# Performance work log

Hardware: AMD Instinct MI355X
Metric: run time of the kernel (lower is better)

The kernel has to match this reference:

```python
import jax, jax.numpy as jnp
import numpy as np

N_NODES = 20000
N_EDGES = 160000
N_GRAPHS = 500
F_IN = 128
HID = 512
N_CLS = 10
N_LAYERS = 3
BN_EPS = 1e-5
BN_BIAS = 1e-4  # BatchNorm1d weight init to 1, bias to 0.0001


def bn(x):
    # training-mode BatchNorm1d with gamma=1, beta=1e-4 (per module init)
    m = jnp.mean(x, axis=0)
    v = jnp.mean((x - m) ** 2, axis=0)
    return (x - m) * jax.lax.rsqrt(v + BN_EPS) + BN_BIAS


def gcn_norm(row, col, edge_weight, num_nodes):
    # add self loops with weight 1, symmetric deg^-1/2 normalization
    loop = jnp.arange(num_nodes)
    r = jnp.concatenate([row, loop])
    c = jnp.concatenate([col, loop])
    w = jnp.concatenate([edge_weight, jnp.ones((num_nodes,), edge_weight.dtype)])
    deg = jax.ops.segment_sum(w, r, num_segments=num_nodes)
    dis = jnp.where(deg > 0, jax.lax.rsqrt(deg), jnp.zeros_like(deg))
    return r, c, dis[r] * w * dis[c]


def gcn(x, W, b, r, c, norm):
    # x@W then gather source feats, scale by norm, scatter-add to targets
    h = x @ W
    out = jax.ops.segment_sum(norm[:, None] * h[c], r, num_segments=x.shape[0])
    return out + b


def readout(x, W1, b1, W2, b2):
    x = bn(x) @ W1 + b1
    x = jax.nn.relu(x)
    x = bn(x) @ W2 + b2
    return jax.nn.log_softmax(x, axis=-1)


def setup_inputs() -> dict:
    key = jax.random.key(0)
    ks = iter(jax.random.split(key, 40))

    def lin(k, fin, fout):
        return jax.random.normal(k, (fin, fout), jnp.float32) * (1.0 / np.sqrt(fin))

    x = jax.random.normal(next(ks), (N_NODES, F_IN), jnp.float32)
    edge_index = jax.random.randint(next(ks), (2, N_EDGES), 0, N_NODES)
    batch = jnp.sort(jax.random.randint(next(ks), (N_NODES,), 0, N_GRAPHS))
    perm = jax.random.permutation(next(ks), N_GRAPHS)

    inp = {"x": x, "edge_index": edge_index, "batch": batch, "perm": perm}
    inp["conv_feat_W"] = lin(next(ks), F_IN, HID)
    inp["conv_feat_b"] = jnp.zeros((HID,), jnp.float32)
    inp["convs_W"] = jax.random.normal(next(ks), (N_LAYERS, HID, HID), jnp.float32) * (1.0 / np.sqrt(HID))
    inp["convs_b"] = jnp.zeros((N_LAYERS, HID), jnp.float32)
    inp["edge_att_W"] = lin(next(ks), 2 * HID, 2)
    inp["edge_att_b"] = jnp.zeros((2,), jnp.float32)
    inp["node_att_W"] = lin(next(ks), HID, 2)
    inp["node_att_b"] = jnp.zeros((2,), jnp.float32)
    inp["ctx_W"] = lin(next(ks), HID, HID)
    inp["ctx_b"] = jnp.zeros((HID,), jnp.float32)
    inp["obj_W"] = lin(next(ks), HID, HID)
    inp["obj_b"] = jnp.zeros((HID,), jnp.float32)
    for tag in ("c", "o", "co"):
        inp[f"fc1_{tag}_W"] = lin(next(ks), HID, HID)
        inp[f"fc1_{tag}_b"] = jnp.zeros((HID,), jnp.float32)
        inp[f"fc2_{tag}_W"] = lin(next(ks), HID, N_CLS)
        inp[f"fc2_{tag}_b"] = jnp.zeros((N_CLS,), jnp.float32)
    return inp


def reference(x, edge_index, batch, perm,
              conv_feat_W, conv_feat_b, convs_W, convs_b,
              edge_att_W, edge_att_b, node_att_W, node_att_b,
              ctx_W, ctx_b, obj_W, obj_b,
              fc1_c_W, fc1_c_b, fc2_c_W, fc2_c_b,
              fc1_o_W, fc1_o_b, fc2_o_W, fc2_o_b,
              fc1_co_W, fc1_co_b, fc2_co_W, fc2_co_b):
    row, col = edge_index[0], edge_index[1]
    n = x.shape[0]

    x = bn(x)
    x = jax.nn.relu(x @ conv_feat_W + conv_feat_b)  # conv_feat has gfn=True: pure linear

    # unweighted symmetric norm, shared by all stacked convs
    r1, c1, nrm1 = gcn_norm(row, col, jnp.ones((row.shape[0],), x.dtype), n)
    for i in range(N_LAYERS):
        x = bn(x)
        x = jax.nn.relu(gcn(x, convs_W[i], convs_b[i], r1, c1, nrm1))

    edge_rep = jnp.concatenate([x[row], x[col]], axis=-1)        # [E, 2H]
    edge_att = jax.nn.softmax(edge_rep @ edge_att_W + edge_att_b, axis=-1)
    node_att = jax.nn.softmax(x @ node_att_W + node_att_b, axis=-1)

    xc = node_att[:, :1] * x
    xo = node_att[:, 1:] * x

    rc, cc, nc = gcn_norm(row, col, edge_att[:, 0], n)
    ro, co_, no_ = gcn_norm(row, col, edge_att[:, 1], n)
    xc = jax.nn.relu(gcn(bn(xc), ctx_W, ctx_b, rc, cc, nc))
    xo = jax.nn.relu(gcn(bn(xo), obj_W, obj_b, ro, co_, no_))

    xc = jax.ops.segment_sum(xc, batch, num_segments=N_GRAPHS)   # global_add_pool
    xo = jax.ops.segment_sum(xo, batch, num_segments=N_GRAPHS)

    xc_logis = readout(xc, fc1_c_W, fc1_c_b, fc2_c_W, fc2_c_b)
    xo_logis = readout(xo, fc1_o_W, fc1_o_b, fc2_o_W, fc2_o_b)
    # cat_or_add == 'add', with_random shuffle realized by perm
    xco_logis = readout(xc[perm] + xo, fc1_co_W, fc1_co_b, fc2_co_W, fc2_co_b)
    return xc_logis, xo_logis, xco_logis
```

## Files before the change

### kernel.cpp

```cpp
#include <hip/hip_runtime.h>
#include <stdint.h>

#define NN 20000
#define NE 160000
#define NG 500
#define FIN 128
#define HID 512
#define NCLS 10
#define BNG 256
#define NB3 32

typedef __attribute__((ext_vector_type(8))) short short8;
typedef __attribute__((ext_vector_type(4))) float f32x4;
typedef __attribute__((ext_vector_type(4))) unsigned short ushort4v;

__device__ __forceinline__ float bf2f(unsigned int u){
  union{unsigned int i; float f;} x; x.i = u<<16; return x.f;
}
__device__ __forceinline__ unsigned short f2bf(float f){
  union{float f; unsigned int i;} x; x.f=f;
  unsigned int r = x.i + 0x7fffu + ((x.i>>16)&1u);
  return (unsigned short)(r>>16);
}
__device__ __forceinline__ unsigned int pk2(float a, float b){
  return (unsigned int)f2bf(a) | ((unsigned int)f2bf(b) << 16);
}

__device__ __forceinline__ void gload16(unsigned short* lds, const unsigned short* g){
  __builtin_amdgcn_global_load_lds((const __attribute__((address_space(1))) unsigned int*)g,
                                   (__attribute__((address_space(3))) unsigned int*)lds,
                                   16, 0, 0);
}

__device__ __forceinline__ void fma8(float* acc, uint4 v, float w){
  acc[0] += w*bf2f(v.x & 0xffffu); acc[1] += w*bf2f(v.x >> 16);
  acc[2] += w*bf2f(v.y & 0xffffu); acc[3] += w*bf2f(v.y >> 16);
  acc[4] += w*bf2f(v.z & 0xffffu); acc[5] += w*bf2f(v.z >> 16);
  acc[6] += w*bf2f(v.w & 0xffffu); acc[7] += w*bf2f(v.w >> 16);
}

__global__ void sentinel_k(float* out){ out[0] = 12345.0f; }

struct W2BT { const float* src[9]; unsigned short* dst[9]; };
__global__ void setup_all(W2BT p, int* __restrict__ cnt, int* __restrict__ fillc,
                          float* __restrict__ degc, float* __restrict__ dego,
                          float* __restrict__ Sc, float* __restrict__ So,
                          float* __restrict__ stats6){
  int idx = blockIdx.x*blockDim.x + threadIdx.x;
  if (idx < FIN*HID + 8*HID*HID){
    int seg, off, K;
    if (idx < FIN*HID){ seg = 0; off = idx; K = FIN; }
    else {
      int r = idx - FIN*HID;
      seg = 1 + (r >> 18); off = r & (HID*HID-1); K = HID;
    }
    int k = off >> 9, n = off & 511;
    p.dst[seg][(size_t)n*K + k] = f2bf(p.src[seg][off]);
  }
  if (idx < NN){ cnt[idx]=0; fillc[idx]=0; degc[idx]=1.0f; dego[idx]=1.0f; Sc[idx]=0.f; So[idx]=0.f; }
  if (idx < 6*1024) stats6[idx] = 0.f;
}

__global__ __launch_bounds__(1024) void bnstats_p(const float* __restrict__ X, int M, int F,
                                                  float* __restrict__ partials){
  __shared__ float lds[1024*9];
  const int t = threadIdx.x;
  const int cg = F >> 2;
  const int cid = t & (cg-1);
  const int rid = t / cg;
  const int rpb = 1024 / cg;
  float s0=0,s1=0,s2=0,s3=0,q0=0,q1=0,q2=0,q3=0;
  const int rowsPer = (M + BNG - 1)/BNG;
  int r0 = blockIdx.x*rowsPer, r1 = r0 + rowsPer; if (r1 > M) r1 = M;
  for (int r = r0 + rid; r < r1; r += rpb){
    float4 v = *(const float4*)&X[(size_t)r*F + cid*4];
    s0+=v.x; q0+=v.x*v.x; s1+=v.y; q1+=v.y*v.y; s2+=v.z; q2+=v.z*v.z; s3+=v.w; q3+=v.w*v.w;
  }
  int base = (rid*cg + cid)*9;
  lds[base+0]=s0; lds[base+1]=s1; lds[base+2]=s2; lds[base+3]=s3;
  lds[base+4]=q0; lds[base+5]=q1; lds[base+6]=q2; lds[base+7]=q3;
  __syncthreads();
  if (t < cg*8){
    int ci = t >> 3, i = t & 7;
    float acc = 0.f;
    for (int g=0; g<rpb; ++g) acc += lds[(g*cg + ci)*9 + i];
    int col = ci*4 + (i & 3);
    partials[(size_t)blockIdx.x*(2*F) + ((i < 4) ? col : F + col)] = acc;
  }
}

__global__ __launch_bounds__(1024) void bnstats_dual(const unsigned short* __restrict__ X,
                                                     const float* __restrict__ na,
                                                     float* __restrict__ partials){
  __shared__ float lds[1024*17];
  const int t = threadIdx.x;
  const int cid = t & 127;
  const int rid = t >> 7;
  float sC[4]={0,0,0,0}, qC[4]={0,0,0,0}, sO[4]={0,0,0,0}, qO[4]={0,0,0,0};
  const int rowsPer = (NN + BNG - 1)/BNG;
  int r0 = blockIdx.x*rowsPer, r1 = r0 + rowsPer; if (r1 > NN) r1 = NN;
  for (int r = r0 + rid; r < r1; r += 8){
    float a0 = na[2*r], a1 = na[2*r+1];
    uint2 u = *(const uint2*)&X[(size_t)r*HID + cid*4];
    float e[4] = {bf2f(u.x & 0xffffu), bf2f(u.x >> 16), bf2f(u.y & 0xffffu), bf2f(u.y >> 16)};
#pragma unroll
    for (int i=0;i<4;i++){
      float vc = e[i]*a0, vo = e[i]*a1;
      sC[i]+=vc; qC[i]+=vc*vc; sO[i]+=vo; qO[i]+=vo*vo;
    }
  }
  int base = (rid*128 + cid)*17;
#pragma unroll
  for (int i=0;i<4;i++){
    lds[base+i]=sC[i]; lds[base+4+i]=qC[i]; lds[base+8+i]=sO[i]; lds[base+12+i]=qO[i];
  }
  __syncthreads();
  for (int idx = t; idx < 2048; idx += 1024){
    int ci = idx >> 4, i = idx & 15;
    float acc = 0.f;
    for (int g=0; g<8; ++g) acc += lds[(g*128 + ci)*17 + i];
    int grp = i >> 2, col = ci*4 + (i & 3);
    partials[(size_t)blockIdx.x*2048 + grp*HID + col] = acc;
  }
}

__global__ void bnfin_red(const float* __restrict__ partials, int stride, int off,
                          int M, int F, float* __restrict__ mstat){
  __shared__ float lds[4][64][2];
  int t = threadIdx.x;
  int cl = t & 63, ch = t >> 6;
  int c = blockIdx.x*64 + cl;
  float s = 0.f, q = 0.f;
  if (c < F){
    for (int b = ch*64; b < ch*64 + 64; ++b){
      s += partials[(size_t)b*stride + off + c];
      q += partials[(size_t)b*stride + off + F + c];
    }
  }
  lds[ch][cl][0] = s; lds[ch][cl][1] = q;
  __syncthreads();
  if (ch == 0 && c < F){
    s = lds[0][cl][0]+lds[1][cl][0]+lds[2][cl][0]+lds[3][cl][0];
    q = lds[0][cl][1]+lds[1][cl][1]+lds[2][cl][1]+lds[3][cl][1];
    float m = s/(float)M;
    float v = q/(float)M - m*m;
    mstat[c] = m;
    mstat[F+c] = rsqrtf(v + 1e-5f);
  }
}

__global__ void bnfin_red2(const float* __restrict__ partials, float* __restrict__ mstatCO){
  __shared__ float lds[4][64][2];
  int t = threadIdx.x;
  int cl = t & 63, ch = t >> 6;
  int c = blockIdx.x*64 + cl;
  int off = blockIdx.y*1024;
  float s = 0.f, q = 0.f;
  for (int b = ch*64; b < ch*64 + 64; ++b){
    s += partials[(size_t)b*2048 + off + c];
    q += partials[(size_t)b*2048 + off + HID + c];
  }
  lds[ch][cl][0] = s; lds[ch][cl][1] = q;
  __syncthreads();
  if (ch == 0){
    s = lds[0][cl][0]+lds[1][cl][0]+lds[2][cl][0]+lds[3][cl][0];
    q = lds[0][cl][1]+lds[1][cl][1]+lds[2][cl][1]+lds[3][cl][1];
    float m = s/(float)NN;
    float v = q/(float)NN - m*m;
    mstatCO[blockIdx.y*1024 + c] = m;
    mstatCO[blockIdx.y*1024 + HID + c] = rsqrtf(v + 1e-5f);
  }
}

__global__ void bncast(const float* __restrict__ X, const float* __restrict__ mstat,
                       int M, int F, unsigned short* __restrict__ out){
  int idx = blockIdx.x*blockDim.x + threadIdx.x;
  int total4 = M*F/4;
  if (idx >= total4) return;
  int base = idx*4;
  int c = base & (F-1);
  float4 v = *(const float4*)&X[base];
  ushort4v o;
  o[0] = f2bf((v.x - mstat[c+0])*mstat[F+c+0] + 1e-4f);
  o[1] = f2bf((v.y - mstat[c+1])*mstat[F+c+1] + 1e-4f);
  o[2] = f2bf((v.z - mstat[c+2])*mstat[F+c+2] + 1e-4f);
  o[3] = f2bf((v.w - mstat[c+3])*mstat[F+c+3] + 1e-4f);
  *(ushort4v*)&out[base] = o;
}

__global__ void csr_count(const int* __restrict__ ei, int* __restrict__ cnt){
  int e = blockIdx.x*blockDim.x + threadIdx.x;
  if (e < NE) atomicAdd(&cnt[ei[e]], 1);
}

__global__ __launch_bounds__(1024) void scan1(const int* __restrict__ cnt, int* __restrict__ rowp,
                                              float* __restrict__ dis1, int* __restrict__ bsum){
  __shared__ int buf[1024];
  int t = threadIdx.x;
  int i = blockIdx.x*1024 + t;
  int v = 0;
  if (i < NN){ v = cnt[i] + 1; dis1[i] = rsqrtf((float)v); }
  buf[t] = v;
  __syncthreads();
  for (int off=1; off<1024; off<<=1){
    int xv = (t >= off) ? buf[t-off] : 0;
    __syncthreads();
    buf[t] += xv;
    __syncthreads();
  }
  if (i < NN) rowp[i+1] = buf[t];
  if (t == 1023) bsum[blockIdx.x] = buf[1023];
}

__global__ __launch_bounds__(1024) void scan3(int* __restrict__ rowp, const int* __restrict__ bsum){
  __shared__ int base;
  int bx = blockIdx.x;
  if (threadIdx.x == 0){
    int a = 0;
    for (int b=0; b<bx; ++b) a += bsum[b];
    base = a;
  }
  __syncthreads();
  int i = bx*1024 + threadIdx.x;
  if (i < NN) rowp[i+1] += base;
  if (i == 0) rowp[0] = 0;
}

__global__ void csr_fill(const int* __restrict__ ei, const int* __restrict__ rowp,
                         const int* __restrict__ cnt, int* __restrict__ fillc,
                         const float* __restrict__ dis1,
                         int* __restrict__ ccol, int* __restrict__ crow, int* __restrict__ ceid,
                         float* __restrict__ w1){
  int id = blockIdx.x*blockDim.x + threadIdx.x;
  if (id < NE){
    int r = ei[id], c = ei[NE + id];
    int pos = atomicAdd(&fillc[r], 1);
    int idx = rowp[r] + pos;
    ccol[idx] = c; crow[idx] = r; ceid[idx] = id;
    w1[idx] = dis1[r]*dis1[c];
  } else if (id < NE + NN){
    int i = id - NE;
    int idx = rowp[i] + cnt[i];
    ccol[idx] = i; crow[idx] = i; ceid[idx] = -1;
    w1[idx] = dis1[i]*dis1[i];
  }
}

__global__ void att_node(const unsigned short* __restrict__ X, const float* __restrict__ nW,
                         const float* __restrict__ nb, const float* __restrict__ eW,
                         float* __restrict__ na, float* __restrict__ eab){
  int wv = blockIdx.x*4 + (threadIdx.x >> 6);
  int l = threadIdx.x & 63;
  if (wv >= NN) return;
  uint4 u = ((const uint4*)(X + (size_t)wv*HID))[l];
  float xv[8] = {bf2f(u.x&0xffffu), bf2f(u.x>>16), bf2f(u.y&0xffffu), bf2f(u.y>>16),
                 bf2f(u.z&0xffffu), bf2f(u.z>>16), bf2f(u.w&0xffffu), bf2f(u.w>>16)};
  float s0=0,s1=0,s2=0,s3=0,s4=0,s5=0;
#pragma unroll
  for (int j=0; j<8; ++j){
    int k = l*8 + j;
    float x = xv[j];
    s0 += x * nW[2*k];       s1 += x * nW[2*k+1];
    s2 += x * eW[2*k];       s3 += x * eW[2*k+1];
    s4 += x * eW[2*(512+k)]; s5 += x * eW[2*(512+k)+1];
  }
  for (int m=1; m<64; m<<=1){
    s0 += __shfl_xor(s0,m); s1 += __shfl_xor(s1,m); s2 += __shfl_xor(s2,m);
    s3 += __shfl_xor(s3,m); s4 += __shfl_xor(s4,m); s5 += __shfl_xor(s5,m);
  }
  if (l == 0){
    float z0 = s0 + nb[0], z1 = s1 + nb[1];
    float mx = fmaxf(z0,z1);
    float e0 = expf(z0-mx), e1 = expf(z1-mx);
    float inv = 1.0f/(e0+e1);
    na[2*wv] = e0*inv; na[2*wv+1] = e1*inv;
    eab[4*wv] = s2; eab[4*wv+1] = s3; eab[4*wv+2] = s4; eab[4*wv+3] = s5;
  }
}

__global__ void att_edge(const int* __restrict__ ei, const float* __restrict__ eab,
                         const float* __restrict__ eb, float* __restrict__ att,
                         float* __restrict__ degc, float* __restrict__ dego){
  int e = blockIdx.x*blockDim.x + threadIdx.x;
  if (e >= NE) return;
  int r = ei[e], c = ei[NE+e];
  float z0 = eab[4*r]   + eab[4*c+2] + eb[0];
  float z1 = eab[4*r+1] + eab[4*c+3] + eb[1];
  float mx = fmaxf(z0,z1);
  float e0 = expf(z0-mx), e1 = expf(z1-mx);
  float inv = 1.0f/(e0+e1);
  float a0 = e0*inv, a1 = e1*inv;
  att[2*e] = a0; att[2*e+1] = a1;
  atomicAdd(&degc[r], a0);
  atomicAdd(&dego[r], a1);
}

__global__ void wco_kernel(const int* __restrict__ crow, const int* __restrict__ ccol,
                           const int* __restrict__ ceid, const float* __restrict__ att,
                           const float* __restrict__ degc, const float* __restrict__ dego,
                           const float* __restrict__ na,
                           float* __restrict__ wcv, float* __restrict__ wov,
                           float* __restrict__ Sc, float* __restrict__ So){
  int j = blockIdx.x*blockDim.x + threadIdx.x;
  if (j >= NE + NN) return;
  int r = crow[j], c = ccol[j], e = ceid[j];
  float a0 = (e < 0) ? 1.0f : att[2*e];
  float a1 = (e < 0) ? 1.0f : att[2*e+1];
  float wc = rsqrtf(degc[r]) * a0 * rsqrtf(degc[c]);
  float wo = rsqrtf(dego[r]) * a1 * rsqrtf(dego[c]);
  wcv[j] = wc * na[2*c];
  wov[j] = wo * na[2*c+1];
  atomicAdd(&Sc[r], wc);
  atomicAdd(&So[r], wo);
}

__global__ __launch_bounds__(256) void aggregate_bn(const unsigned short* __restrict__ A,
                                                    const int* __restrict__ rowp,
                                                    const int* __restrict__ ccol,
                                                    const float* __restrict__ wv,
                                                    const float* __restrict__ stats,
                                                    float invM,
                                                    unsigned short* __restrict__ out){
  int row = blockIdx.x*4 + (threadIdx.x >> 6);
  int l = threadIdx.x & 63;
  const uint4* Av = (const uint4*)A;
  int s = rowp[row], e = rowp[row+1];
  float acc[8] = {0,0,0,0,0,0,0,0};
  float sw = 0.f;
  int j = s;
  for (; j+1 < e; j += 2){
    int c0 = ccol[j], c1 = ccol[j+1];
    float w0 = wv[j], w1 = wv[j+1];
    uint4 v0 = Av[(size_t)c0*64 + l];
    uint4 v1 = Av[(size_t)c1*64 + l];
    fma8(acc, v0, w0);
    fma8(acc, v1, w1);
    sw += w0 + w1;
  }
  if (j < e){
    uint4 v = Av[(size_t)ccol[j]*64 + l];
    fma8(acc, v, wv[j]);
    sw += wv[j];
  }
  float g[8];
#pragma unroll
  for (int i=0;i<8;i++){
    int c = l*8 + i;
    float m = stats[c]*invM;
    float rs = rsqrtf(stats[512+c]*invM - m*m + 1e-5f);
    g[i] = rs*acc[i] + sw*(1e-4f - m*rs);
  }
  uint4 o;
  o.x = pk2(g[0],g[1]); o.y = pk2(g[2],g[3]); o.z = pk2(g[4],g[5]); o.w = pk2(g[6],g[7]);
  ((uint4*)out)[(size_t)row*64 + l] = o;
}

__global__ __launch_bounds__(256) void aggregate_dual(const unsigned short* __restrict__ A,
                                                      const int* __restrict__ rowp,
                                                      const int* __restrict__ ccol,
                                                      const float* __restrict__ wc,
                                                      const float* __restrict__ wo,
                                                      const float* __restrict__ Sc,
                                                      const float* __restrict__ So,
                                                      const float* __restrict__ mstatCO,
                                                      unsigned short* __restrict__ outC,
                                                      unsigned short* __restrict__ outO){
  int row = blockIdx.x*4 + (threadIdx.x >> 6);
  int l = threadIdx.x & 63;
  const uint4* Av = (const uint4*)A;
  int s = rowp[row], e = rowp[row+1];
  float aC[8] = {0,0,0,0,0,0,0,0};
  float aO[8] = {0,0,0,0,0,0,0,0};
  int j = s;
  for (; j+1 < e; j += 2){
    int c0 = ccol[j], c1 = ccol[j+1];
    float wc0 = wc[j], wc1 = wc[j+1];
    float wo0 = wo[j], wo1 = wo[j+1];
    uint4 v0 = Av[(size_t)c0*64 + l];
    uint4 v1 = Av[(size_t)c1*64 + l];
    fma8(aC, v0, wc0); fma8(aO, v0, wo0);
    fma8(aC, v1, wc1); fma8(aO, v1, wo1);
  }
  if (j < e){
    uint4 v = Av[(size_t)ccol[j]*64 + l];
    fma8(aC, v, wc[j]); fma8(aO, v, wo[j]);
  }
  float ScR = Sc[row], SoR = So[row];
  float gC[8], gO[8];
#pragma unroll
  for (int i=0;i<8;i++){
    int c = l*8 + i;
    float mc = mstatCO[c],      rc = mstatCO[512+c];
    float mo = mstatCO[1024+c], ro = mstatCO[1536+c];
    gC[i] = rc*aC[i] + ScR*(1e-4f - mc*rc);
    gO[i] = ro*aO[i] + SoR*(1e-4f - mo*ro);
  }
  uint4 oc, oo;
  oc.x = pk2(gC[0],gC[1]); oc.y = pk2(gC[2],gC[3]); oc.z = pk2(gC[4],gC[5]); oc.w = pk2(gC[6],gC[7]);
  oo.x = pk2(gO[0],gO[1]); oo.y = pk2(gO[2],gO[3]); oo.z = pk2(gO[4],gO[5]); oo.w = pk2(gO[6],gO[7]);
  ((uint4*)outC)[(size_t)row*64 + l] = oc;
  ((uint4*)outO)[(size_t)row*64 + l] = oo;
}

__global__ __launch_bounds__(256) void gemm_bt(const unsigned short* __restrict__ A,
                                               const unsigned short* __restrict__ Bt,
                                               unsigned short* __restrict__ O,
                                               const float* __restrict__ bias,
                                               float* __restrict__ stats,
                                               int M, int K, int relu){
  __shared__ unsigned short As[2][128*32];
  __shared__ unsigned short Bs[2][128*32];
  const int tid = threadIdx.x;
  const int w = tid >> 6, l = tid & 63;
  const int m0 = blockIdx.x*128, n0 = blockIdx.y*128;
  const int wm = w >> 1, wn = w & 1;
  const int lr = l & 15, lh = l >> 4;

  f32x4 acc[4][4];
#pragma unroll
  for (int i=0;i<4;i++)
#pragma unroll
    for (int j=0;j<4;j++) acc[i][j] = 0.0f;

  const int q0 = w*2, q1 = w*2+1;
  const int sub = l >> 2;
  const int kc  = (l & 3)*8;
  int ma0 = m0 + q0*16 + sub; if (ma0 >= M) ma0 = M-1;
  int ma1 = m0 + q1*16 + sub; if (ma1 >= M) ma1 = M-1;
  const int nb0 = n0 + q0*16 + sub;
  const int nb1 = n0 + q1*16 + sub;
  const unsigned short* Ar0 = A + (size_t)ma0*K + kc;
  const unsigned short* Ar1 = A + (size_t)ma1*K + kc;
  const unsigned short* Br0 = Bt + (size_t)nb0*K + kc;
  const unsigned short* Br1 = Bt + (size_t)nb1*K + kc;

  const int NT = K >> 5;
  gload16(&As[0][q0*512], Ar0);
  gload16(&As[0][q1*512], Ar1);
  gload16(&Bs[0][q0*512], Br0);
  gload16(&Bs[0][q1*512], Br1);
  __syncthreads();
  int cur = 0;
  for (int t=0; t<NT; ++t){
    if (t+1 < NT){
      int k1 = (t+1) << 5;
      gload16(&As[cur^1][q0*512], Ar0 + k1);
      gload16(&As[cur^1][q1*512], Ar1 + k1);
      gload16(&Bs[cur^1][q0*512], Br0 + k1);
      gload16(&Bs[cur^1][q1*512], Br1 + k1);
    }
    short8 af[4], bfr[4];
#pragma unroll
    for (int fm=0; fm<4; ++fm) af[fm]  = *(const short8*)&As[cur][(wm*64 + fm*16 + lr)*32 + lh*8];
#pragma unroll
    for (int fn=0; fn<4; ++fn) bfr[fn] = *(const short8*)&Bs[cur][(wn*64 + fn*16 + lr)*32 + lh*8];
#pragma unroll
    for (int fm=0; fm<4; ++fm)
#pragma unroll
      for (int fn=0; fn<4; ++fn)
        acc[fm][fn] = __builtin_amdgcn_mfma_f32_16x16x32_bf16(af[fm], bfr[fn], acc[fm][fn], 0, 0, 0);
    __syncthreads();
    cur ^= 1;
  }
  float bv[4], cs[4]={0,0,0,0}, cq[4]={0,0,0,0};
  int col[4];
#pragma unroll
  for (int fn=0; fn<4; ++fn){ col[fn] = n0 + wn*64 + fn*16 + lr; bv[fn] = bias[col[fn]]; }
#pragma unroll
  for (int fm=0; fm<4; ++fm){
#pragma unroll
    for (int j=0; j<4; ++j){
      int row = m0 + wm*64 + fm*16 + lh*4 + j;
      if (row < M){
#pragma unroll
        for (int fn=0; fn<4; ++fn){
          float v = acc[fm][fn][j] + bv[fn];
          if (relu) v = fmaxf(v, 0.f);
          O[(size_t)row*HID + col[fn]] = f2bf(v);
          cs[fn] += v; cq[fn] += v*v;
        }
      }
    }
  }
  if (stats){
#pragma unroll
    for (int m=16; m<64; m<<=1){
#pragma unroll
      for (int fn=0; fn<4; ++fn){ cs[fn] += __shfl_xor(cs[fn], m); cq[fn] += __shfl_xor(cq[fn], m); }
    }
    if (lh == 0){
#pragma unroll
      for (int fn=0; fn<4; ++fn){
        atomicAdd(&stats[col[fn]], cs[fn]);
        atomicAdd(&stats[512+col[fn]], cq[fn]);
      }
    }
  }
}

struct FC1P { const unsigned short* Bt[3]; const float* bias[3]; };
__global__ __launch_bounds__(256) void gemm_fc1(const unsigned short* __restrict__ A, FC1P p,
                                                unsigned short* __restrict__ O,
                                                float* __restrict__ statsB){
  __shared__ unsigned short As[2][128*32];
  __shared__ unsigned short Bs[2][128*32];
  const int tid = threadIdx.x;
  const int w = tid >> 6, l = tid & 63;
  const int m0 = blockIdx.x*128, n0 = blockIdx.y*128;
  const int branch = blockIdx.x >> 2;
  const unsigned short* Bt = p.Bt[branch];
  const float* bias = p.bias[branch];
  float* stats = statsB + branch*1024;
  const int K = HID;
  const int wm = w >> 1, wn = w & 1;
  const int lr = l & 15, lh = l >> 4;

  f32x4 acc[4][4];
#pragma unroll
  for (int i=0;i<4;i++)
#pragma unroll
    for (int j=0;j<4;j++) acc[i][j] = 0.0f;

  const int q0 = w*2, q1 = w*2+1;
  const int sub = l >> 2;
  const int kc  = (l & 3)*8;
  const int ma0 = m0 + q0*16 + sub;
  const int ma1 = m0 + q1*16 + sub;
  const int nb0 = n0 + q0*16 + sub;
  const int nb1 = n0 + q1*16 + sub;
  const unsigned short* Ar0 = A + (size_t)ma0*K + kc;
  const unsigned short* Ar1 = A + (size_t)ma1*K + kc;
  const unsigned short* Br0 = Bt + (size_t)nb0*K + kc;
  const unsigned short* Br1 = Bt + (size_t)nb1*K + kc;

  const int NT = K >> 5;
  gload16(&As[0][q0*512], Ar0);
  gload16(&As[0][q1*512], Ar1);
  gload16(&Bs[0][q0*512], Br0);
  gload16(&Bs[0][q1*512], Br1);
  __syncthreads();
  int cur = 0;
  for (int t=0; t<NT; ++t){
    if (t+1 < NT){
      int k1 = (t+1) << 5;
      gload16(&As[cur^1][q0*512], Ar0 + k1);
      gload16(&As[cur^1][q1*512], Ar1 + k1);
      gload16(&Bs[cur^1][q0*512], Br0 + k1);
      gload16(&Bs[cur^1][q1*512], Br1 + k1);
    }
    short8 af[4], bfr[4];
#pragma unroll
    for (int fm=0; fm<4; ++fm) af[fm]  = *(const short8*)&As[cur][(wm*64 + fm*16 + lr)*32 + lh*8];
#pragma unroll
    for (int fn=0; fn<4; ++fn) bfr[fn] = *(const short8*)&Bs[cur][(wn*64 + fn*16 + lr)*32 + lh*8];
#pragma unroll
    for (int fm=0; fm<4; ++fm)
#pragma unroll
      for (int fn=0; fn<4; ++fn)
        acc[fm][fn] = __builtin_amdgcn_mfma_f32_16x16x32_bf16(af[fm], bfr[fn], acc[fm][fn], 0, 0, 0);
    __syncthreads();
    cur ^= 1;
  }
  float bv[4], cs[4]={0,0,0,0}, cq[4]={0,0,0,0};
  int col[4];
#pragma unroll
  for (int fn=0; fn<4; ++fn){ col[fn] = n0 + wn*64 + fn*16 + lr; bv[fn] = bias[col[fn]]; }
#pragma unroll
  for (int fm=0; fm<4; ++fm){
#pragma unroll
    for (int j=0; j<4; ++j){
      int row = m0 + wm*64 + fm*16 + lh*4 + j;
      bool real = (row & 511) < NG;
#pragma unroll
      for (int fn=0; fn<4; ++fn){
        float v = fmaxf(acc[fm][fn][j] + bv[fn], 0.f);
        O[(size_t)row*HID + col[fn]] = f2bf(v);
        if (real){ cs[fn] += v; cq[fn] += v*v; }
      }
    }
  }
#pragma unroll
  for (int m=16; m<64; m<<=1){
#pragma unroll
    for (int fn=0; fn<4; ++fn){ cs[fn] += __shfl_xor(cs[fn], m); cq[fn] += __shfl_xor(cq[fn], m); }
  }
  if (lh == 0){
#pragma unroll
    for (int fn=0; fn<4; ++fn){
      atomicAdd(&stats[col[fn]], cs[fn]);
      atomicAdd(&stats[512+col[fn]], cq[fn]);
    }
  }
}

__global__ void pool2(const unsigned short* __restrict__ XC, const unsigned short* __restrict__ XO,
                      const int* __restrict__ batch, float* __restrict__ gc, float* __restrict__ go){
  int g = blockIdx.x;
  int t = threadIdx.x;
  const unsigned short* X = blockIdx.y ? XO : XC;
  float* out = blockIdx.y ? go : gc;
  int lo = 0, hi = NN;
  while (lo < hi){ int mid = (lo+hi) >> 1; if (batch[mid] < g) lo = mid+1; else hi = mid; }
  int s = lo;
  lo = 0; hi = NN;
  while (lo < hi){ int mid = (lo+hi) >> 1; if (batch[mid] < g+1) lo = mid+1; else hi = mid; }
  int e = lo;
  float a0 = 0.f, a1 = 0.f;
  for (int i=s; i<e; ++i){
    unsigned int v = *(const unsigned int*)&X[(size_t)i*HID + t*2];
    a0 += bf2f(v & 0xffffu); a1 += bf2f(v >> 16);
  }
  out[(size_t)g*HID + t*2]     = a0;
  out[(size_t)g*HID + t*2 + 1] = a1;
}

__global__ __launch_bounds__(256) void bnstats3(const float* __restrict__ gc, const float* __restrict__ go,
                                                const int* __restrict__ perm, float* __restrict__ partials){
  __shared__ float lds[256*9];
  int br = blockIdx.y;
  int t = threadIdx.x;
  int cid = t & 127, rid = t >> 7;
  float s[4]={0,0,0,0}, q[4]={0,0,0,0};
  const int rowsPer = (NG + NB3 - 1)/NB3;
  int r0 = blockIdx.x*rowsPer, r1 = r0 + rowsPer; if (r1 > NG) r1 = NG;
  for (int r = r0 + rid; r < r1; r += 2){
    float4 v;
    if (br == 0)      v = *(const float4*)&gc[(size_t)r*HID + cid*4];
    else if (br == 1) v = *(const float4*)&go[(size_t)r*HID + cid*4];
    else {
      int ps = perm[r];
      float4 a = *(const float4*)&gc[(size_t)ps*HID + cid*4];
      float4 b = *(const float4*)&go[(size_t)r*HID + cid*4];
      v = make_float4(a.x+b.x, a.y+b.y, a.z+b.z, a.w+b.w);
    }
    float e[4] = {v.x, v.y, v.z, v.w};
#pragma unroll
    for (int i=0;i<4;i++){ s[i]+=e[i]; q[i]+=e[i]*e[i]; }
  }
  int base = (rid*128 + cid)*9;
#pragma unroll
  for (int i=0;i<4;i++){ lds[base+i]=s[i]; lds[base+4+i]=q[i]; }
  __syncthreads();
  for (int o = t; o < 1024; o += 256){
    int issq = o >> 9, col = o & 511;
    int ci = col >> 2, i = col & 3;
    float acc = lds[(0*128 + ci)*9 + issq*4 + i] + lds[(1*128 + ci)*9 + issq*4 + i];
    partials[(size_t)(br*NB3 + blockIdx.x)*1024 + issq*512 + col] = acc;
  }
}

__global__ void bnfin3(const float* __restrict__ partials, float* __restrict__ mstat3){
  __shared__ float lds[4][64][2];
  int t = threadIdx.x;
  int cl = t & 63, ch = t >> 6;
  int c = blockIdx.x*64 + cl;
  int br = blockIdx.y;
  float s = 0.f, q = 0.f;
  for (int b = ch*8; b < ch*8 + 8; ++b){
    s += partials[(size_t)(br*NB3 + b)*1024 + c];
    q += partials[(size_t)(br*NB3 + b)*1024 + 512 + c];
  }
  lds[ch][cl][0] = s; lds[ch][cl][1] = q;
  __syncthreads();
  if (ch == 0){
    s = lds[0][cl][0]+lds[1][cl][0]+lds[2][cl][0]+lds[3][cl][0];
    q = lds[0][cl][1]+lds[1][cl][1]+lds[2][cl][1]+lds[3][cl][1];
    float m = s/(float)NG;
    float v = q/(float)NG - m*m;
    mstat3[br*1024 + c] = m;
    mstat3[br*1024 + 512 + c] = rsqrtf(v + 1e-5f);
  }
}

__global__ void bncast3(const float* __restrict__ gc, const float* __restrict__ go,
                        const int* __restrict__ perm, const float* __restrict__ mstat3,
                        unsigned short* __restrict__ out){
  int idx = blockIdx.x*blockDim.x + threadIdx.x;
  if (idx >= 1536*128) return;
  int r = idx >> 7;
  int cg = idx & 127;
  int br = r >> 9, lr = r & 511;
  ushort4v o;
  if (lr >= NG){ o[0]=0; o[1]=0; o[2]=0; o[3]=0; }
  else {
    float4 v;
    if (br == 0)      v = *(const float4*)&gc[(size_t)lr*HID + cg*4];
    else if (br == 1) v = *(const float4*)&go[(size_t)lr*HID + cg*4];
    else {
      int ps = perm[lr];
      float4 a = *(const float4*)&gc[(size_t)ps*HID + cg*4];
      float4 b = *(const float4*)&go[(size_t)lr*HID + cg*4];
      v = make_float4(a.x+b.x, a.y+b.y, a.z+b.z, a.w+b.w);
    }
    const float* ms = mstat3 + br*1024;
    int c = cg*4;
    o[0] = f2bf((v.x - ms[c+0])*ms[512+c+0] + 1e-4f);
    o[1] = f2bf((v.y - ms[c+1])*ms[512+c+1] + 1e-4f);
    o[2] = f2bf((v.z - ms[c+2])*ms[512+c+2] + 1e-4f);
    o[3] = f2bf((v.w - ms[c+3])*ms[512+c+3] + 1e-4f);
  }
  *(ushort4v*)&out[(size_t)r*HID + cg*4] = o;
}

struct ROP { const float* W2[3]; const float* b2[3]; };
__global__ void readout_final3(const unsigned short* __restrict__ T, const float* __restrict__ statsB,
                               float invM, ROP p, float* __restrict__ out){
  int g = blockIdx.x;
  int br = blockIdx.y;
  int l = threadIdx.x;
  const float* stats = statsB + br*1024;
  const float* W2 = p.W2[br];
  const float* b2 = p.b2[br];
  float acc[NCLS];
#pragma unroll
  for (int c=0; c<NCLS; ++c) acc[c] = 0.f;
  uint4 u = ((const uint4*)(T + (size_t)(br*512 + g)*HID))[l];
  float xv[8] = {bf2f(u.x&0xffffu), bf2f(u.x>>16), bf2f(u.y&0xffffu), bf2f(u.y>>16),
                 bf2f(u.z&0xffffu), bf2f(u.z>>16), bf2f(u.w&0xffffu), bf2f(u.w>>16)};
#pragma unroll
  for (int j=0; j<8; ++j){
    int k = l*8 + j;
    float m = stats[k]*invM;
    float rs = rsqrtf(stats[512+k]*invM - m*m + 1e-5f);
    float v = (xv[j] - m)*rs + 1e-4f;
#pragma unroll
    for (int c=0; c<NCLS; ++c) acc[c] += v * W2[k*NCLS + c];
  }
  for (int m=1; m<64; m<<=1){
#pragma unroll
    for (int c=0; c<NCLS; ++c) acc[c] += __shfl_xor(acc[c], m);
  }
  if (l == 0){
    float z[NCLS];
    float mx = -1e30f;
#pragma unroll
    for (int c=0; c<NCLS; ++c){ z[c] = acc[c] + b2[c]; mx = fmaxf(mx, z[c]); }
    float s = 0.f;
#pragma unroll
    for (int c=0; c<NCLS; ++c) s += expf(z[c]-mx);
    float lse = mx + logf(s);
#pragma unroll
    for (int c=0; c<NCLS; ++c) out[(size_t)(br*NG + g)*NCLS + c] = z[c] - lse;
  }
}

extern "C" void kernel_launch(void* const* d_in, const int* in_sizes, int n_in,
                              void* d_out, int out_size, void* d_ws, size_t ws_size,
                              hipStream_t stream){
  (void)in_sizes; (void)n_in; (void)out_size;
  const float* x      = (const float*)d_in[0];
  const int*   ei     = (const int*)d_in[1];
  const int*   batch  = (const int*)d_in[2];
  const int*   perm   = (const int*)d_in[3];
  const float* convfW = (const float*)d_in[4];
  const float* convfB = (const float*)d_in[5];
  const float* convsW = (const float*)d_in[6];
  const float* convsB = (const float*)d_in[7];
  const float* eattW  = (const float*)d_in[8];
  const float* eattB  = (const float*)d_in[9];
  const float* nattW  = (const float*)d_in[10];
  const float* nattB  = (const float*)d_in[11];
  const float* ctxW   = (const float*)d_in[12];
  const float* ctxB   = (const float*)d_in[13];
  const float* objW   = (const float*)d_in[14];
  const float* objB   = (const float*)d_in[15];
  const float* fc1W[3] = {(const float*)d_in[16], (const float*)d_in[20], (const float*)d_in[24]};
  const float* fc1B[3] = {(const float*)d_in[17], (const float*)d_in[21], (const float*)d_in[25]};
  const float* fc2W[3] = {(const float*)d_in[18], (const float*)d_in[22], (const float*)d_in[26]};
  const float* fc2B[3] = {(const float*)d_in[19], (const float*)d_in[23], (const float*)d_in[27]};
  float* out = (float*)d_out;

  char* p = (char*)d_ws;
  auto alloc = [&](size_t bytes)->char*{ char* r = p; p += (bytes + 255) & ~((size_t)255); return r; };
  const int T = NE + NN;
  unsigned short* Xbf = (unsigned short*)alloc((size_t)NN*HID*2);
  unsigned short* Gbf = (unsigned short*)alloc((size_t)NN*HID*2);
  unsigned short* GbfO= (unsigned short*)alloc((size_t)NN*HID*2);
  unsigned short* Abf = (unsigned short*)alloc((size_t)NN*FIN*2);
  unsigned short* WtF = (unsigned short*)alloc((size_t)HID*FIN*2);
  unsigned short* WtL = (unsigned short*)alloc((size_t)3*HID*HID*2);
  unsigned short* WtC = (unsigned short*)alloc((size_t)HID*HID*2);
  unsigned short* WtO = (unsigned short*)alloc((size_t)HID*HID*2);
  unsigned short* WtR = (unsigned short*)alloc((size_t)3*HID*HID*2);
  int* cnt   = (int*)alloc((size_t)NN*4);
  int* fillc = (int*)alloc((size_t)NN*4);
  int* rowp  = (int*)alloc((size_t)(NN+1)*4);
  int* bsum  = (int*)alloc(32*4);
  int* ccol  = (int*)alloc((size_t)T*4);
  int* crow  = (int*)alloc((size_t)T*4);
  int* ceid  = (int*)alloc((size_t)T*4);
  float* w1  = (float*)alloc((size_t)T*4);
  float* wcv = (float*)alloc((size_t)T*4);
  float* wov = (float*)alloc((size_t)T*4);
  float* dis1 = (float*)alloc((size_t)NN*4);
  float* degc = (float*)alloc((size_t)NN*4);
  float* dego = (float*)alloc((size_t)NN*4);
  float* Sc   = (float*)alloc((size_t)NN*4);
  float* So   = (float*)alloc((size_t)NN*4);
  float* stats6 = (float*)alloc(6*1024*4);
  float* mstat  = (float*)alloc(2*HID*4);
  float* mstatCO= (float*)alloc(2*1024*4);
  float* mstat3 = (float*)alloc(3*1024*4);
  float* na   = (float*)alloc((size_t)NN*2*4);
  float* eab  = (float*)alloc((size_t)NN*4*4);
  float* att  = (float*)alloc((size_t)NE*2*4);
  float* gc   = (float*)alloc((size_t)NG*HID*4);
  float* go   = (float*)alloc((size_t)NG*HID*4);
  float* part = (float*)alloc((size_t)BNG*2048*4);
  if ((size_t)(p - (char*)d_ws) > ws_size){
    sentinel_k<<<1,1,0,stream>>>(out);
    return;
  }
  unsigned short* Abf3 = Abf;
  unsigned short* Gbf3 = GbfO;
  const float invNN = 1.0f/(float)NN;
  const float invNG = 1.0f/(float)NG;

  W2BT wp;
  wp.src[0]=convfW; wp.dst[0]=WtF;
  for (int i=0;i<3;i++){ wp.src[1+i]=convsW+(size_t)i*HID*HID; wp.dst[1+i]=WtL+(size_t)i*HID*HID; }
  wp.src[4]=ctxW; wp.dst[4]=WtC;
  wp.src[5]=objW; wp.dst[5]=WtO;
  for (int i=0;i<3;i++){ wp.src[6+i]=fc1W[i]; wp.dst[6+i]=WtR+(size_t)i*HID*HID; }
  setup_all<<<(FIN*HID + 8*HID*HID + 255)/256, 256, 0, stream>>>(wp, cnt, fillc, degc, dego, Sc, So, stats6);

  csr_count<<<(NE+255)/256,256,0,stream>>>(ei, cnt);
  scan1<<<(NN+1023)/1024,1024,0,stream>>>(cnt, rowp, dis1, bsum);
  scan3<<<(NN+1023)/1024,1024,0,stream>>>(rowp, bsum);
  csr_fill<<<(T+255)/256,256,0,stream>>>(ei, rowp, cnt, fillc, dis1, ccol, crow, ceid, w1);

  bnstats_p<<<BNG,1024,0,stream>>>(x, NN, FIN, part);
  bnfin_red<<<(FIN+63)/64,256,0,stream>>>(part, 2*FIN, 0, NN, FIN, mstat);
  bncast<<<((NN*FIN/4)+255)/256,256,0,stream>>>(x, mstat, NN, FIN, Abf);
  gemm_bt<<<dim3((NN+127)/128,4),256,0,stream>>>(Abf, WtF, Xbf, convfB, stats6, NN, FIN, 1);

  for (int i=0;i<3;i++){
    aggregate_bn<<<NN/4,256,0,stream>>>(Xbf, rowp, ccol, w1, stats6 + i*1024, invNN, Gbf);
    gemm_bt<<<dim3((NN+127)/128,4),256,0,stream>>>(Gbf, WtL+(size_t)i*HID*HID, Xbf,
                                                   convsB+(size_t)i*HID,
                                                   (i<2) ? (stats6 + (i+1)*1024) : nullptr,
                                                   NN, HID, 1);
  }

  att_node<<<(NN+3)/4,256,0,stream>>>(Xbf, nattW, nattB, eattW, na, eab);
  att_edge<<<(NE+255)/256,256,0,stream>>>(ei, eab, eattB, att, degc, dego);
  wco_kernel<<<(T+255)/256,256,0,stream>>>(crow, ccol, ceid, att, degc, dego, na, wcv, wov, Sc, So);

  bnstats_dual<<<BNG,1024,0,stream>>>(Xbf, na, part);
  bnfin_red2<<<dim3(8,2),256,0,stream>>>(part, mstatCO);
  aggregate_dual<<<NN/4,256,0,stream>>>(Xbf, rowp, ccol, wcv, wov, Sc, So, mstatCO, Gbf, GbfO);
  gemm_bt<<<dim3((NN+127)/128,4),256,0,stream>>>(Gbf, WtC, Xbf, ctxB, nullptr, NN, HID, 1);
  gemm_bt<<<dim3((NN+127)/128,4),256,0,stream>>>(GbfO, WtO, Gbf, objB, nullptr, NN, HID, 1);
  pool2<<<dim3(NG,2),256,0,stream>>>(Xbf, Gbf, batch, gc, go);

  bnstats3<<<dim3(NB3,3),256,0,stream>>>(gc, go, perm, part);
  bnfin3<<<dim3(8,3),256,0,stream>>>(part, mstat3);
  bncast3<<<(1536*128+255)/256,256,0,stream>>>(gc, go, perm, mstat3, Abf3);
  FC1P fp;
  for (int i=0;i<3;i++){ fp.Bt[i] = WtR+(size_t)i*HID*HID; fp.bias[i] = fc1B[i]; }
  gemm_fc1<<<dim3(12,4),256,0,stream>>>(Abf3, fp, Gbf3, stats6 + 3*1024);
  ROP rp;
  for (int i=0;i<3;i++){ rp.W2[i] = fc2W[i]; rp.b2[i] = fc2B[i]; }
  readout_final3<<<dim3(NG,3),64,0,stream>>>(Gbf3, stats6 + 3*1024, invNG, rp, out);
}
```

Measured before the change: 482.5 us.

## Pack CSR col/weight pairs, unroll aggregation, merge ctx/obj GEMMs, relax GEMM barriers

```diff
diff --git a/kernel.cpp b/kernel.cpp
--- a/kernel.cpp
+++ b/kernel.cpp
@@ -230,28 +230,31 @@
                          const int* __restrict__ cnt, int* __restrict__ fillc,
                          const float* __restrict__ dis1,
                          int* __restrict__ ccol, int* __restrict__ crow, int* __restrict__ ceid,
-                         float* __restrict__ w1){
+                         int2* __restrict__ cw1){
   int id = blockIdx.x*blockDim.x + threadIdx.x;
   if (id < NE){
     int r = ei[id], c = ei[NE + id];
     int pos = atomicAdd(&fillc[r], 1);
     int idx = rowp[r] + pos;
     ccol[idx] = c; crow[idx] = r; ceid[idx] = id;
-    w1[idx] = dis1[r]*dis1[c];
+    cw1[idx] = make_int2(c, __float_as_int(dis1[r]*dis1[c]));
   } else if (id < NE + NN){
     int i = id - NE;
     int idx = rowp[i] + cnt[i];
     ccol[idx] = i; crow[idx] = i; ceid[idx] = -1;
-    w1[idx] = dis1[i]*dis1[i];
+    cw1[idx] = make_int2(i, __float_as_int(dis1[i]*dis1[i]));
   }
 }
 
 __global__ void att_node(const unsigned short* __restrict__ X, const float* __restrict__ nW,
                          const float* __restrict__ nb, const float* __restrict__ eW,
                          float* __restrict__ na, float* __restrict__ eab){
-  int wv = blockIdx.x*4 + (threadIdx.x >> 6);
-  int l = threadIdx.x & 63;
-  if (wv >= NN) return;
+  __shared__ float wnl[1024], wet[1024], web[1024];
+  int t = threadIdx.x;
+  for (int i=t; i<1024; i+=256){ wnl[i]=nW[i]; wet[i]=eW[i]; web[i]=eW[1024+i]; }
+  __syncthreads();
+  int wv = blockIdx.x*4 + (t >> 6);
+  int l = t & 63;
   uint4 u = ((const uint4*)(X + (size_t)wv*HID))[l];
   float xv[8] = {bf2f(u.x&0xffffu), bf2f(u.x>>16), bf2f(u.y&0xffffu), bf2f(u.y>>16),
                  bf2f(u.z&0xffffu), bf2f(u.z>>16), bf2f(u.w&0xffffu), bf2f(u.w>>16)};
@@ -260,9 +263,9 @@
   for (int j=0; j<8; ++j){
     int k = l*8 + j;
     float x = xv[j];
-    s0 += x * nW[2*k];       s1 += x * nW[2*k+1];
-    s2 += x * eW[2*k];       s3 += x * eW[2*k+1];
-    s4 += x * eW[2*(512+k)]; s5 += x * eW[2*(512+k)+1];
+    s0 += x * wnl[2*k];   s1 += x * wnl[2*k+1];
+    s2 += x * wet[2*k];   s3 += x * wet[2*k+1];
+    s4 += x * web[2*k];   s5 += x * web[2*k+1];
   }
   for (int m=1; m<64; m<<=1){
     s0 += __shfl_xor(s0,m); s1 += __shfl_xor(s1,m); s2 += __shfl_xor(s2,m);
@@ -316,8 +319,7 @@
 
 __global__ __launch_bounds__(256) void aggregate_bn(const unsigned short* __restrict__ A,
                                                     const int* __restrict__ rowp,
-                                                    const int* __restrict__ ccol,
-                                                    const float* __restrict__ wv,
+                                                    const int2* __restrict__ cw,
                                                     const float* __restrict__ stats,
                                                     float invM,
                                                     unsigned short* __restrict__ out){
@@ -328,19 +330,23 @@
   float acc[8] = {0,0,0,0,0,0,0,0};
   float sw = 0.f;
   int j = s;
-  for (; j+1 < e; j += 2){
-    int c0 = ccol[j], c1 = ccol[j+1];
-    float w0 = wv[j], w1 = wv[j+1];
-    uint4 v0 = Av[(size_t)c0*64 + l];
-    uint4 v1 = Av[(size_t)c1*64 + l];
-    fma8(acc, v0, w0);
-    fma8(acc, v1, w1);
-    sw += w0 + w1;
-  }
-  if (j < e){
-    uint4 v = Av[(size_t)ccol[j]*64 + l];
-    fma8(acc, v, wv[j]);
-    sw += wv[j];
+  for (; j+3 < e; j += 4){
+    int2 p0 = cw[j], p1 = cw[j+1], p2 = cw[j+2], p3 = cw[j+3];
+    float w0 = __int_as_float(p0.y), w1 = __int_as_float(p1.y);
+    float w2 = __int_as_float(p2.y), w3 = __int_as_float(p3.y);
+    uint4 v0 = Av[(size_t)p0.x*64 + l];
+    uint4 v1 = Av[(size_t)p1.x*64 + l];
+    uint4 v2 = Av[(size_t)p2.x*64 + l];
+    uint4 v3 = Av[(size_t)p3.x*64 + l];
+    fma8(acc, v0, w0); fma8(acc, v1, w1); fma8(acc, v2, w2); fma8(acc, v3, w3);
+    sw += w0 + w1 + w2 + w3;
+  }
+  for (; j < e; ++j){
+    int2 p = cw[j];
+    float w = __int_as_float(p.y);
+    uint4 v = Av[(size_t)p.x*64 + l];
+    fma8(acc, v, w);
+    sw += w;
   }
   float g[8];
 #pragma unroll
@@ -372,16 +378,20 @@
   float aC[8] = {0,0,0,0,0,0,0,0};
   float aO[8] = {0,0,0,0,0,0,0,0};
   int j = s;
-  for (; j+1 < e; j += 2){
-    int c0 = ccol[j], c1 = ccol[j+1];
-    float wc0 = wc[j], wc1 = wc[j+1];
-    float wo0 = wo[j], wo1 = wo[j+1];
+  for (; j+3 < e; j += 4){
+    int c0 = ccol[j], c1 = ccol[j+1], c2 = ccol[j+2], c3 = ccol[j+3];
+    float wc0=wc[j], wc1=wc[j+1], wc2=wc[j+2], wc3=wc[j+3];
+    float wo0=wo[j], wo1=wo[j+1], wo2=wo[j+2], wo3=wo[j+3];
     uint4 v0 = Av[(size_t)c0*64 + l];
     uint4 v1 = Av[(size_t)c1*64 + l];
+    uint4 v2 = Av[(size_t)c2*64 + l];
+    uint4 v3 = Av[(size_t)c3*64 + l];
     fma8(aC, v0, wc0); fma8(aO, v0, wo0);
     fma8(aC, v1, wc1); fma8(aO, v1, wo1);
-  }
-  if (j < e){
+    fma8(aC, v2, wc2); fma8(aO, v2, wo2);
+    fma8(aC, v3, wc3); fma8(aO, v3, wo3);
+  }
+  for (; j < e; ++j){
     uint4 v = Av[(size_t)ccol[j]*64 + l];
     fma8(aC, v, wc[j]); fma8(aO, v, wo[j]);
   }
@@ -407,12 +417,18 @@
                                                unsigned short* __restrict__ O,
                                                const float* __restrict__ bias,
                                                float* __restrict__ stats,
-                                               int M, int K, int relu){
+                                               int M, int K, int relu, int split,
+                                               const unsigned short* A2,
+                                               const unsigned short* Bt2,
+                                               unsigned short* O2,
+                                               const float* bias2){
   __shared__ unsigned short As[2][128*32];
   __shared__ unsigned short Bs[2][128*32];
   const int tid = threadIdx.x;
   const int w = tid >> 6, l = tid & 63;
-  const int m0 = blockIdx.x*128, n0 = blockIdx.y*128;
+  int bx = blockIdx.x;
+  if (split && bx >= split){ A = A2; Bt = Bt2; O = O2; bias = bias2; bx -= split; }
+  const int m0 = bx*128, n0 = blockIdx.y*128;
   const int wm = w >> 1, wn = w & 1;
   const int lr = l & 15, lh = l >> 4;
 
@@ -439,7 +455,6 @@
   gload16(&As[0][q1*512], Ar1);
   gload16(&Bs[0][q0*512], Br0);
   gload16(&Bs[0][q1*512], Br1);
-  __syncthreads();
   int cur = 0;
   for (int t=0; t<NT; ++t){
     if (t+1 < NT){
@@ -448,7 +463,12 @@
       gload16(&As[cur^1][q1*512], Ar1 + k1);
       gload16(&Bs[cur^1][q0*512], Br0 + k1);
       gload16(&Bs[cur^1][q1*512], Br1 + k1);
-    }
+      asm volatile("s_waitcnt vmcnt(4)" ::: "memory");
+    } else {
+      asm volatile("s_waitcnt vmcnt(0)" ::: "memory");
+    }
+    __builtin_amdgcn_s_barrier();
+    asm volatile("" ::: "memory");
     short8 af[4], bfr[4];
 #pragma unroll
     for (int fm=0; fm<4; ++fm) af[fm]  = *(const short8*)&As[cur][(wm*64 + fm*16 + lr)*32 + lh*8];
@@ -459,7 +479,9 @@
 #pragma unroll
       for (int fn=0; fn<4; ++fn)
         acc[fm][fn] = __builtin_amdgcn_mfma_f32_16x16x32_bf16(af[fm], bfr[fn], acc[fm][fn], 0, 0, 0);
-    __syncthreads();
+    asm volatile("" ::: "memory");
+    __builtin_amdgcn_s_barrier();
+    asm volatile("" ::: "memory");
     cur ^= 1;
   }
   float bv[4], cs[4]={0,0,0,0}, cq[4]={0,0,0,0};
@@ -538,7 +560,6 @@
   gload16(&As[0][q1*512], Ar1);
   gload16(&Bs[0][q0*512], Br0);
   gload16(&Bs[0][q1*512], Br1);
-  __syncthreads();
   int cur = 0;
   for (int t=0; t<NT; ++t){
     if (t+1 < NT){
@@ -547,7 +568,12 @@
       gload16(&As[cur^1][q1*512], Ar1 + k1);
       gload16(&Bs[cur^1][q0*512], Br0 + k1);
       gload16(&Bs[cur^1][q1*512], Br1 + k1);
-    }
+      asm volatile("s_waitcnt vmcnt(4)" ::: "memory");
+    } else {
+      asm volatile("s_waitcnt vmcnt(0)" ::: "memory");
+    }
+    __builtin_amdgcn_s_barrier();
+    asm volatile("" ::: "memory");
     short8 af[4], bfr[4];
 #pragma unroll
     for (int fm=0; fm<4; ++fm) af[fm]  = *(const short8*)&As[cur][(wm*64 + fm*16 + lr)*32 + lh*8];
@@ -558,7 +584,9 @@
 #pragma unroll
       for (int fn=0; fn<4; ++fn)
         acc[fm][fn] = __builtin_amdgcn_mfma_f32_16x16x32_bf16(af[fm], bfr[fn], acc[fm][fn], 0, 0, 0);
-    __syncthreads();
+    asm volatile("" ::: "memory");
+    __builtin_amdgcn_s_barrier();
+    asm volatile("" ::: "memory");
     cur ^= 1;
   }
   float bv[4], cs[4]={0,0,0,0}, cq[4]={0,0,0,0};
@@ -776,6 +804,7 @@
   unsigned short* Xbf = (unsigned short*)alloc((size_t)NN*HID*2);
   unsigned short* Gbf = (unsigned short*)alloc((size_t)NN*HID*2);
   unsigned short* GbfO= (unsigned short*)alloc((size_t)NN*HID*2);
+  unsigned short* XbfO= (unsigned short*)alloc((size_t)NN*HID*2);
   unsigned short* Abf = (unsigned short*)alloc((size_t)NN*FIN*2);
   unsigned short* WtF = (unsigned short*)alloc((size_t)HID*FIN*2);
   unsigned short* WtL = (unsigned short*)alloc((size_t)3*HID*HID*2);
@@ -789,7 +818,7 @@
   int* ccol  = (int*)alloc((size_t)T*4);
   int* crow  = (int*)alloc((size_t)T*4);
   int* ceid  = (int*)alloc((size_t)T*4);
-  float* w1  = (float*)alloc((size_t)T*4);
+  int2* cw1  = (int2*)alloc((size_t)T*8);
   float* wcv = (float*)alloc((size_t)T*4);
   float* wov = (float*)alloc((size_t)T*4);
   float* dis1 = (float*)alloc((size_t)NN*4);
@@ -827,31 +856,35 @@
   csr_count<<<(NE+255)/256,256,0,stream>>>(ei, cnt);
   scan1<<<(NN+1023)/1024,1024,0,stream>>>(cnt, rowp, dis1, bsum);
   scan3<<<(NN+1023)/1024,1024,0,stream>>>(rowp, bsum);
-  csr_fill<<<(T+255)/256,256,0,stream>>>(ei, rowp, cnt, fillc, dis1, ccol, crow, ceid, w1);
+  csr_fill<<<(T+255)/256,256,0,stream>>>(ei, rowp, cnt, fillc, dis1, ccol, crow, ceid, cw1);
 
   bnstats_p<<<BNG,1024,0,stream>>>(x, NN, FIN, part);
   bnfin_red<<<(FIN+63)/64,256,0,stream>>>(part, 2*FIN, 0, NN, FIN, mstat);
   bncast<<<((NN*FIN/4)+255)/256,256,0,stream>>>(x, mstat, NN, FIN, Abf);
-  gemm_bt<<<dim3((NN+127)/128,4),256,0,stream>>>(Abf, WtF, Xbf, convfB, stats6, NN, FIN, 1);
+  gemm_bt<<<dim3((NN+127)/128,4),256,0,stream>>>(Abf, WtF, Xbf, convfB, stats6, NN, FIN, 1,
+                                                 0, nullptr, nullptr, nullptr, nullptr);
 
   for (int i=0;i<3;i++){
-    aggregate_bn<<<NN/4,256,0,stream>>>(Xbf, rowp, ccol, w1, stats6 + i*1024, invNN, Gbf);
+    aggregate_bn<<<NN/4,256,0,stream>>>(Xbf, rowp, cw1, stats6 + i*1024, invNN, Gbf);
     gemm_bt<<<dim3((NN+127)/128,4),256,0,stream>>>(Gbf, WtL+(size_t)i*HID*HID, Xbf,
                                                    convsB+(size_t)i*HID,
                                                    (i<2) ? (stats6 + (i+1)*1024) : nullptr,
-                                                   NN, HID, 1);
-  }
-
-  att_node<<<(NN+3)/4,256,0,stream>>>(Xbf, nattW, nattB, eattW, na, eab);
+                                                   NN, HID, 1, 0, nullptr, nullptr, nullptr, nullptr);
+  }
+
+  att_node<<<NN/4,256,0,stream>>>(Xbf, nattW, nattB, eattW, na, eab);
   att_edge<<<(NE+255)/256,256,0,stream>>>(ei, eab, eattB, att, degc, dego);
   wco_kernel<<<(T+255)/256,256,0,stream>>>(crow, ccol, ceid, att, degc, dego, na, wcv, wov, Sc, So);
 
   bnstats_dual<<<BNG,1024,0,stream>>>(Xbf, na, part);
   bnfin_red2<<<dim3(8,2),256,0,stream>>>(part, mstatCO);
   aggregate_dual<<<NN/4,256,0,stream>>>(Xbf, rowp, ccol, wcv, wov, Sc, So, mstatCO, Gbf, GbfO);
-  gemm_bt<<<dim3((NN+127)/128,4),256,0,stream>>>(Gbf, WtC, Xbf, ctxB, nullptr, NN, HID, 1);
-  gemm_bt<<<dim3((NN+127)/128,4),256,0,stream>>>(GbfO, WtO, Gbf, objB, nullptr, NN, HID, 1);
-  pool2<<<dim3(NG,2),256,0,stream>>>(Xbf, Gbf, batch, gc, go);
+  {
+    const int gx = (NN+127)/128;
+    gemm_bt<<<dim3(2*gx,4),256,0,stream>>>(Gbf, WtC, Xbf, ctxB, nullptr, NN, HID, 1,
+                                           gx, GbfO, WtO, XbfO, objB);
+  }
+  pool2<<<dim3(NG,2),256,0,stream>>>(Xbf, XbfO, batch, gc, go);
 
   bnstats3<<<dim3(NB3,3),256,0,stream>>>(gc, go, perm, part);
   bnfin3<<<dim3(8,3),256,0,stream>>>(part, mstat3);
```

Measured after the change: 476.6 us. No clear change (-1.2%).
